# Kernel tuning notes

Measured on AMD Instinct MI355X. Metric: run time of the kernel, lower is better.

Reference implementation:

```python
import jax, jax.numpy as jnp
import numpy as np

OUT = 7  # output_size of AdaptiveMaxPool2d


def _roi_pool(images, rois, roi_idx):
    # images: [N,C,H,W]; rois: [R,4] rel coords (x1,y1,x2,y2); roi_idx: [R]
    n, c, h, w = images.shape
    x1 = jnp.floor(rois[:, 0] * w).astype(jnp.int32)
    y1 = jnp.floor(rois[:, 1] * h).astype(jnp.int32)
    x2 = jnp.ceil(rois[:, 2] * w).astype(jnp.int32)
    y2 = jnp.ceil(rois[:, 3] * h).astype(jnp.int32)
    Hr = y2 - y1  # per-ROI crop height
    Wr = x2 - x1  # per-ROI crop width

    feats = images[roi_idx]  # [R,C,H,W] gather per-ROI source image
    hh = jnp.arange(h)
    ww = jnp.arange(w)
    neg = jnp.finfo(images.dtype).min

    # Adaptive max pool is separable: max over row-bins, then col-bins.
    # PyTorch adaptive bins over a region of size L: [floor(i*L/OUT), ceil((i+1)*L/OUT))
    rows = []
    for i in range(OUT):  # small fixed loop over output rows
        s = y1 + (i * Hr) // OUT
        e = y1 + ((i + 1) * Hr + OUT - 1) // OUT  # ceil
        m = (hh[None, :] >= s[:, None]) & (hh[None, :] < e[:, None])  # [R,H]
        rows.append(jnp.max(jnp.where(m[:, None, :, None], feats, neg), axis=2))  # [R,C,W]
    rowp = jnp.stack(rows, axis=2)  # [R,C,OUT,W]

    cols = []
    for j in range(OUT):  # small fixed loop over output cols
        s = x1 + (j * Wr) // OUT
        e = x1 + ((j + 1) * Wr + OUT - 1) // OUT
        m = (ww[None, :] >= s[:, None]) & (ww[None, :] < e[:, None])  # [R,W]
        cols.append(jnp.max(jnp.where(m[:, None, None, :], rowp, neg), axis=3))  # [R,C,OUT]
    return jnp.stack(cols, axis=3)  # [R,C,OUT,OUT]


def setup_inputs() -> dict:
    key = jax.random.key(0)
    k1, k2, k3 = jax.random.split(key, 3)
    N, C, H, W, R = 8, 256, 56, 56, 256
    images = jax.random.normal(k1, (N, C, H, W), dtype=jnp.float32)
    # build valid boxes: x1<x2, y1<y2 in [0,1]
    pts = jax.random.uniform(k2, (R, 2, 2), dtype=jnp.float32)
    lo = jnp.min(pts, axis=1)
    hi = jnp.max(pts, axis=1)
    rois = jnp.stack([lo[:, 0], lo[:, 1], hi[:, 0], hi[:, 1]], axis=1)  # [R,4]
    roi_idx = jax.random.randint(k3, (R,), 0, N)
    return {"images": images, "rois": rois, "roi_idx": roi_idx}


def reference(images, rois, roi_idx):
    return _roi_pool(images, rois, roi_idx)
```

## Files before the change

### kernel.cpp

```cpp
#include <hip/hip_runtime.h>

#define OUTS 7
#define CC 256
#define HH 56
#define WW 56
#define PX (HH * WW)
#define PSTRIDE 57
#define SSTRIDE 57
#define SPLIT 2
#define MAXROI 80

typedef _Float16 half2_t __attribute__((ext_vector_type(2)));

__device__ __forceinline__ half2_t h2max(half2_t a, unsigned b) {
    return __builtin_elementwise_max(a, __builtin_bit_cast(half2_t, b));
}
__device__ __forceinline__ unsigned h2bits(half2_t a) {
    return __builtin_bit_cast(unsigned, a);
}

__global__ __launch_bounds__(256) void roipool_kernel(
    const float* __restrict__ images, const float* __restrict__ rois,
    const int* __restrict__ roi_idx, float* __restrict__ out, int R)
{
    __shared__ __align__(16) uint4 plane8[PSTRIDE * HH];
    __shared__ __align__(16) uint4 scratch[4 * OUTS * SSTRIDE];
    __shared__ int list[MAXROI];
    __shared__ unsigned short ys[MAXROI * 7];
    __shared__ unsigned short xs[MAXROI * 7];
    __shared__ unsigned char  xb[MAXROI];
    __shared__ int cnt;

    const int b  = blockIdx.x;
    const int s  = b & 1;
    const int q  = b >> 1;
    const int n  = q >> 5;
    const int c0 = (q & 31) * 8;
    const int t  = threadIdx.x;

    if (t < 64) {
        int base = 0;
        #pragma unroll
        for (int k = 0; k < 4; ++k) {
            int r = k * 64 + t;
            bool match = (r < R) && (roi_idx[r] == n);
            unsigned long long mask = __ballot(match);
            int pos = base + __popcll(mask & ((1ULL << t) - 1ULL));
            if (match && pos < MAXROI) list[pos] = r;
            base += __popcll(mask);
        }
        int count0 = (base < MAXROI) ? base : MAXROI;
        if (t == 0) cnt = count0;

        for (int e = t; e < count0 * 7; e += 64) {
            int m = e / 7, i = e - m * 7;
            int r = list[m];
            float4 rv = reinterpret_cast<const float4*>(rois)[r];
            int x1 = (int)floorf(rv.x * (float)WW);
            int y1 = (int)floorf(rv.y * (float)HH);
            int x2 = (int)ceilf (rv.z * (float)WW);
            int y2 = (int)ceilf (rv.w * (float)HH);
            int Hr = y2 - y1, Wr = x2 - x1;
            int sy  = y1 + (i * Hr) / 7;
            int ey  = y1 + ((i + 1) * Hr + 6) / 7;
            int sxr = (i * Wr) / 7;
            int exr = ((i + 1) * Wr + 6) / 7;
            ys[m * 7 + i] = (unsigned short)(sy | (ey << 8));
            xs[m * 7 + i] = (unsigned short)(sxr | (exr << 8));
            if (i == 0) xb[m] = (unsigned char)x1;
        }
    }

    const float* base0 = images + (size_t)(n * CC + c0) * PX;
    #pragma unroll
    for (int k = 0; k < 4; ++k) {
        int idx = t + k * 256;
        if (idx < PX / 4) {
            float4 f0 = reinterpret_cast<const float4*>(base0 + 0 * PX)[idx];
            float4 f1 = reinterpret_cast<const float4*>(base0 + 1 * PX)[idx];
            float4 f2 = reinterpret_cast<const float4*>(base0 + 2 * PX)[idx];
            float4 f3 = reinterpret_cast<const float4*>(base0 + 3 * PX)[idx];
            float4 f4 = reinterpret_cast<const float4*>(base0 + 4 * PX)[idx];
            float4 f5 = reinterpret_cast<const float4*>(base0 + 5 * PX)[idx];
            float4 f6 = reinterpret_cast<const float4*>(base0 + 6 * PX)[idx];
            float4 f7 = reinterpret_cast<const float4*>(base0 + 7 * PX)[idx];
            int y  = idx / 14;
            int x0 = (idx - y * 14) * 4;
            uint4* dst = &plane8[y * PSTRIDE + x0];
            #pragma unroll
            for (int p = 0; p < 4; ++p) {
                half2_t h01 = { (_Float16)(&f0.x)[p], (_Float16)(&f1.x)[p] };
                half2_t h23 = { (_Float16)(&f2.x)[p], (_Float16)(&f3.x)[p] };
                half2_t h45 = { (_Float16)(&f4.x)[p], (_Float16)(&f5.x)[p] };
                half2_t h67 = { (_Float16)(&f6.x)[p], (_Float16)(&f7.x)[p] };
                dst[p] = make_uint4(h2bits(h01), h2bits(h23), h2bits(h45), h2bits(h67));
            }
        }
    }
    __syncthreads();

    const int count = cnt;
    const int wv   = t >> 6;
    const int lane = t & 63;
    const int ii   = lane / 7;
    const int jj   = lane - ii * 7;
    uint4* const scr = &scratch[wv * (OUTS * SSTRIDE)];
    const half2_t NEG = { (_Float16)-65504.0f, (_Float16)-65504.0f };

    for (int m = (wv << 1) + s; m < count; m += SPLIT * 4) {
        int r  = list[m];
        int x1 = xb[m];
        int xcol = min(x1 + lane, WW - 1);
        int scol = min(lane, SSTRIDE - 1);

        #pragma unroll
        for (int i = 0; i < 7; ++i) {
            int yse = ys[m * 7 + i];
            int sy = yse & 255, ey = yse >> 8;
            half2_t m01 = NEG, m23 = NEG, m45 = NEG, m67 = NEG;
            const uint4* p = plane8 + sy * PSTRIDE + xcol;
            for (int y = sy; y < ey; ++y) {
                uint4 v = *p;  p += PSTRIDE;
                m01 = h2max(m01, v.x);
                m23 = h2max(m23, v.y);
                m45 = h2max(m45, v.z);
                m67 = h2max(m67, v.w);
            }
            scr[i * SSTRIDE + scol] =
                make_uint4(h2bits(m01), h2bits(m23), h2bits(m45), h2bits(m67));
        }

        if (lane < OUTS * OUTS) {
            int xse = xs[m * 7 + jj];
            int sx = xse & 255, ex = xse >> 8;
            half2_t a01 = NEG, a23 = NEG, a45 = NEG, a67 = NEG;
            const uint4* p = scr + ii * SSTRIDE + sx;
            for (int x = sx; x < ex; ++x) {
                uint4 v = *p++;
                a01 = h2max(a01, v.x);
                a23 = h2max(a23, v.y);
                a45 = h2max(a45, v.z);
                a67 = h2max(a67, v.w);
            }
            size_t o = ((size_t)r * CC + c0) * (OUTS * OUTS) + lane;
            out[o]            = (float)a01.x;
            out[o + 49]       = (float)a01.y;
            out[o + 2 * 49]   = (float)a23.x;
            out[o + 3 * 49]   = (float)a23.y;
            out[o + 4 * 49]   = (float)a45.x;
            out[o + 5 * 49]   = (float)a45.y;
            out[o + 6 * 49]   = (float)a67.x;
            out[o + 7 * 49]   = (float)a67.y;
        }
    }
}

extern "C" void kernel_launch(void* const* d_in, const int* in_sizes, int n_in,
                              void* d_out, int out_size, void* d_ws, size_t ws_size,
                              hipStream_t stream) {
    const float* images  = (const float*)d_in[0];
    const float* rois    = (const float*)d_in[1];
    const int*   roi_idx = (const int*)d_in[2];
    float* out = (float*)d_out;

    int R = in_sizes[2];
    int N = in_sizes[0] / (CC * PX);

    int grid = N * (CC / 8) * SPLIT;
    roipool_kernel<<<grid, 256, 0, stream>>>(images, rois, roi_idx, out, R);
}
```

Measured before the change: 95.13 us.

## Pack 4 channels per block in fp16 planes and unroll pooling loops by two

Each block now handles 4 channels instead of 8, which doubles the grid and halves the fp16 shared-memory plane (uint2 per pixel, stride 58). All global loads for the block are issued before any conversion so they overlap. The row and column max loops are unrolled by two, clamping the second read to the last index. The cost is that each block rebuilds the ROI list and per-ROI bin tables for half as many channels, so that setup work is duplicated more often.

```diff
diff --git a/kernel.cpp b/kernel.cpp
--- a/kernel.cpp
+++ b/kernel.cpp
@@ -5,7 +5,7 @@
 #define HH 56
 #define WW 56
 #define PX (HH * WW)
-#define PSTRIDE 57
+#define STRIDE 58
 #define SSTRIDE 57
 #define SPLIT 2
 #define MAXROI 80
@@ -23,8 +23,8 @@
     const float* __restrict__ images, const float* __restrict__ rois,
     const int* __restrict__ roi_idx, float* __restrict__ out, int R)
 {
-    __shared__ __align__(16) uint4 plane8[PSTRIDE * HH];
-    __shared__ __align__(16) uint4 scratch[4 * OUTS * SSTRIDE];
+    __shared__ __align__(16) uint2 plane2[STRIDE * HH];
+    __shared__ __align__(16) uint2 scratch[4 * OUTS * SSTRIDE];
     __shared__ int list[MAXROI];
     __shared__ unsigned short ys[MAXROI * 7];
     __shared__ unsigned short xs[MAXROI * 7];
@@ -34,8 +34,8 @@
     const int b  = blockIdx.x;
     const int s  = b & 1;
     const int q  = b >> 1;
-    const int n  = q >> 5;
-    const int c0 = (q & 31) * 8;
+    const int n  = q >> 6;
+    const int c0 = (q & 63) * 4;
     const int t  = threadIdx.x;
 
     if (t < 64) {
@@ -72,29 +72,36 @@
     }
 
     const float* base0 = images + (size_t)(n * CC + c0) * PX;
+    float4 ra[4], rb[4], rc[4], rd[4];
     #pragma unroll
     for (int k = 0; k < 4; ++k) {
         int idx = t + k * 256;
         if (idx < PX / 4) {
-            float4 f0 = reinterpret_cast<const float4*>(base0 + 0 * PX)[idx];
-            float4 f1 = reinterpret_cast<const float4*>(base0 + 1 * PX)[idx];
-            float4 f2 = reinterpret_cast<const float4*>(base0 + 2 * PX)[idx];
-            float4 f3 = reinterpret_cast<const float4*>(base0 + 3 * PX)[idx];
-            float4 f4 = reinterpret_cast<const float4*>(base0 + 4 * PX)[idx];
-            float4 f5 = reinterpret_cast<const float4*>(base0 + 5 * PX)[idx];
-            float4 f6 = reinterpret_cast<const float4*>(base0 + 6 * PX)[idx];
-            float4 f7 = reinterpret_cast<const float4*>(base0 + 7 * PX)[idx];
+            ra[k] = reinterpret_cast<const float4*>(base0)[idx];
+            rb[k] = reinterpret_cast<const float4*>(base0 + PX)[idx];
+            rc[k] = reinterpret_cast<const float4*>(base0 + 2 * PX)[idx];
+            rd[k] = reinterpret_cast<const float4*>(base0 + 3 * PX)[idx];
+        }
+    }
+    #pragma unroll
+    for (int k = 0; k < 4; ++k) {
+        int idx = t + k * 256;
+        if (idx < PX / 4) {
+            const float* ap = &ra[k].x; const float* bp = &rb[k].x;
+            const float* cp = &rc[k].x; const float* dp = &rd[k].x;
             int y  = idx / 14;
             int x0 = (idx - y * 14) * 4;
-            uint4* dst = &plane8[y * PSTRIDE + x0];
+            unsigned lo[4], hi[4];
             #pragma unroll
             for (int p = 0; p < 4; ++p) {
-                half2_t h01 = { (_Float16)(&f0.x)[p], (_Float16)(&f1.x)[p] };
-                half2_t h23 = { (_Float16)(&f2.x)[p], (_Float16)(&f3.x)[p] };
-                half2_t h45 = { (_Float16)(&f4.x)[p], (_Float16)(&f5.x)[p] };
-                half2_t h67 = { (_Float16)(&f6.x)[p], (_Float16)(&f7.x)[p] };
-                dst[p] = make_uint4(h2bits(h01), h2bits(h23), h2bits(h45), h2bits(h67));
+                half2_t l = { (_Float16)ap[p], (_Float16)bp[p] };
+                half2_t h = { (_Float16)cp[p], (_Float16)dp[p] };
+                lo[p] = __builtin_bit_cast(unsigned, l);
+                hi[p] = __builtin_bit_cast(unsigned, h);
             }
+            uint4* dst = reinterpret_cast<uint4*>(&plane2[y * STRIDE + x0]);
+            dst[0] = make_uint4(lo[0], hi[0], lo[1], hi[1]);
+            dst[1] = make_uint4(lo[2], hi[2], lo[3], hi[3]);
         }
     }
     __syncthreads();
@@ -104,12 +111,12 @@
     const int lane = t & 63;
     const int ii   = lane / 7;
     const int jj   = lane - ii * 7;
-    uint4* const scr = &scratch[wv * (OUTS * SSTRIDE)];
+    uint2* const scr = &scratch[wv * (OUTS * SSTRIDE)];
     const half2_t NEG = { (_Float16)-65504.0f, (_Float16)-65504.0f };
 
     for (int m = (wv << 1) + s; m < count; m += SPLIT * 4) {
-        int r  = list[m];
-        int x1 = xb[m];
+        int r    = list[m];
+        int x1   = xb[m];
         int xcol = min(x1 + lane, WW - 1);
         int scol = min(lane, SSTRIDE - 1);
 
@@ -117,40 +124,32 @@
         for (int i = 0; i < 7; ++i) {
             int yse = ys[m * 7 + i];
             int sy = yse & 255, ey = yse >> 8;
-            half2_t m01 = NEG, m23 = NEG, m45 = NEG, m67 = NEG;
-            const uint4* p = plane8 + sy * PSTRIDE + xcol;
-            for (int y = sy; y < ey; ++y) {
-                uint4 v = *p;  p += PSTRIDE;
-                m01 = h2max(m01, v.x);
-                m23 = h2max(m23, v.y);
-                m45 = h2max(m45, v.z);
-                m67 = h2max(m67, v.w);
+            half2_t m01 = NEG, m23 = NEG;
+            for (int y = sy; y < ey; y += 2) {
+                uint2 v0 = plane2[y * STRIDE + xcol];
+                uint2 v1 = plane2[min(y + 1, ey - 1) * STRIDE + xcol];
+                m01 = h2max(h2max(m01, v0.x), v1.x);
+                m23 = h2max(h2max(m23, v0.y), v1.y);
             }
-            scr[i * SSTRIDE + scol] =
-                make_uint4(h2bits(m01), h2bits(m23), h2bits(m45), h2bits(m67));
+            scr[i * SSTRIDE + scol] = make_uint2(h2bits(m01), h2bits(m23));
         }
 
         if (lane < OUTS * OUTS) {
             int xse = xs[m * 7 + jj];
             int sx = xse & 255, ex = xse >> 8;
-            half2_t a01 = NEG, a23 = NEG, a45 = NEG, a67 = NEG;
-            const uint4* p = scr + ii * SSTRIDE + sx;
-            for (int x = sx; x < ex; ++x) {
-                uint4 v = *p++;
-                a01 = h2max(a01, v.x);
-                a23 = h2max(a23, v.y);
-                a45 = h2max(a45, v.z);
-                a67 = h2max(a67, v.w);
+            half2_t a01 = NEG, a23 = NEG;
+            const uint2* p = scr + ii * SSTRIDE;
+            for (int x = sx; x < ex; x += 2) {
+                uint2 v0 = p[x];
+                uint2 v1 = p[min(x + 1, ex - 1)];
+                a01 = h2max(h2max(a01, v0.x), v1.x);
+                a23 = h2max(h2max(a23, v0.y), v1.y);
             }
             size_t o = ((size_t)r * CC + c0) * (OUTS * OUTS) + lane;
-            out[o]            = (float)a01.x;
-            out[o + 49]       = (float)a01.y;
-            out[o + 2 * 49]   = (float)a23.x;
-            out[o + 3 * 49]   = (float)a23.y;
-            out[o + 4 * 49]   = (float)a45.x;
-            out[o + 5 * 49]   = (float)a45.y;
-            out[o + 6 * 49]   = (float)a67.x;
-            out[o + 7 * 49]   = (float)a67.y;
+            out[o]       = (float)a01.x;
+            out[o + 49]  = (float)a01.y;
+            out[o + 98]  = (float)a23.x;
+            out[o + 147] = (float)a23.y;
         }
     }
 }
@@ -166,6 +165,6 @@
     int R = in_sizes[2];
     int N = in_sizes[0] / (CC * PX);
 
-    int grid = N * (CC / 8) * SPLIT;
+    int grid = N * (CC / 4) * SPLIT;
     roipool_kernel<<<grid, 256, 0, stream>>>(images, rois, roi_idx, out, R);
 }
```

New measurement: 99.22 us. 1.04x slower.
